# Optimization experiments

Hardware: AMD Instinct MI355X
Metric: run time of the kernel (lower is better)

The kernel has to match this reference:

```python
import jax, jax.numpy as jnp
import numpy as np

EPS = 1e-08

def quantize_weights(w):
    # absmean ternary quantization: round(w/delta) clipped to {-1,0,1}, rescaled by delta
    delta = jnp.mean(jnp.abs(w)) + EPS
    w_quant = jnp.clip(jnp.round(w / delta), -1.0, 1.0)
    return w_quant * delta

def setup_inputs() -> dict:
    key = jax.random.key(0)
    k1, k2 = jax.random.split(key)
    B, T, IN, OUT = 8, 16, 4096, 11008
    x = jax.random.normal(k1, (B, T, IN), dtype=jnp.float32)
    weight = jax.random.normal(k2, (OUT, IN), dtype=jnp.float32)
    bias = jnp.zeros((OUT,), dtype=jnp.float32)
    return {"x": x, "weight": weight, "bias": bias}

def reference(x, weight, bias):
    w_quant = quantize_weights(weight)
    # F.linear: x @ w_quant.T + bias
    out = jnp.einsum("bti,oi->bto", x, w_quant) + bias
    return out
```

## Files before the change

### kernel.cpp

```cpp
#include <hip/hip_runtime.h>
#include <hip/hip_bf16.h>

typedef __bf16 bf16x8 __attribute__((ext_vector_type(8)));
typedef float f32x4 __attribute__((ext_vector_type(4)));
typedef unsigned short ushort8 __attribute__((ext_vector_type(8)));

constexpr int M = 128;
constexpr int K = 4096;
constexpr int N = 11008;
constexpr int BN = 32;
constexpr int BK = 64;
constexpr long long NW = (long long)N * K;
constexpr int RBLK = 2048;

constexpr size_t PART_OFF = 0;
constexpr size_t XBF_OFF  = 8192;
constexpr size_t P0_OFF   = XBF_OFF + (size_t)M * K * 2;
constexpr size_t PSZ      = (size_t)M * N * sizeof(float);
constexpr size_t P1_OFF   = P0_OFF + PSZ;
constexpr size_t WS_NEED  = P1_OFF + PSZ;

__device__ __forceinline__ unsigned short f2bf_bits(float f) {
    unsigned int u = __builtin_bit_cast(unsigned int, f);
    u += 0x7FFFu + ((u >> 16) & 1u);
    return (unsigned short)(u >> 16);
}

template <bool CVT>
__global__ __launch_bounds__(256) void absmean_partial(const float* __restrict__ w,
                                                       const float* __restrict__ x,
                                                       float* __restrict__ partials,
                                                       unsigned short* __restrict__ xbf)
{
    const int gtid = blockIdx.x * blockDim.x + threadIdx.x;
    if (CVT && gtid < M * K / 8) {
        const float4* xp = (const float4*)x + (size_t)gtid * 2;
        float4 a = xp[0], b = xp[1];
        ushort8 o;
        o[0] = f2bf_bits(a.x); o[1] = f2bf_bits(a.y);
        o[2] = f2bf_bits(a.z); o[3] = f2bf_bits(a.w);
        o[4] = f2bf_bits(b.x); o[5] = f2bf_bits(b.y);
        o[6] = f2bf_bits(b.z); o[7] = f2bf_bits(b.w);
        *(ushort8*)(xbf + (size_t)gtid * 8) = o;
    }
    const int n4 = (int)(NW / 4);
    const float4* w4 = (const float4*)w;
    float s0 = 0.f, s1 = 0.f, s2 = 0.f, s3 = 0.f;
    for (int i = gtid; i < n4; i += gridDim.x * blockDim.x) {
        float4 v = w4[i];
        s0 += fabsf(v.x); s1 += fabsf(v.y); s2 += fabsf(v.z); s3 += fabsf(v.w);
    }
    float s = (s0 + s1) + (s2 + s3);
#pragma unroll
    for (int off = 32; off > 0; off >>= 1) s += __shfl_down(s, off, 64);
    __shared__ float red[4];
    if ((threadIdx.x & 63) == 0) red[threadIdx.x >> 6] = s;
    __syncthreads();
    if (threadIdx.x == 0)
        partials[blockIdx.x] = (red[0] + red[1]) + (red[2] + red[3]);
}

template <int KSTEPS, bool DIRECT>
__global__ __launch_bounds__(256) void bitlinear_gemm(
    const void* __restrict__ Xsrc, const float* __restrict__ W,
    const float* __restrict__ bias, const float* __restrict__ partials,
    float* __restrict__ dbase)
{
    constexpr int LDSW = 72;
    __shared__ __attribute__((aligned(16))) unsigned short xs[2][M * LDSW];
    __shared__ __attribute__((aligned(16))) unsigned short wsm[2][BN * LDSW];

    const int tid = threadIdx.x;
    const int lane = tid & 63;
    const int wid = tid >> 6;
    const int wm = wid >> 1;
    const int wn = wid & 1;
    const int cgrp = lane >> 4;
    const int l15 = lane & 15;
    const int n0 = blockIdx.x * BN;
    const int kk0 = DIRECT ? 0 : blockIdx.y * KSTEPS;

    const int sr = tid >> 3;
    const int sc = tid & 7;
    const int K4 = K / 4;

    const float4* wsrc = (const float4*)(W + (size_t)(n0 + sr) * K) + sc * 2;
    const unsigned short* xb = (const unsigned short*)Xsrc;
    const float4* xf = (const float4*)Xsrc;

    float4 wr0, wr1;
    ushort8 xr[4];

    auto issue = [&](int t) {
        const int g = kk0 + t;
        wr0 = wsrc[g * 16];
        wr1 = wsrc[g * 16 + 1];
#pragma unroll
        for (int it = 0; it < 4; ++it) {
            if (!DIRECT) {
                xr[it] = *(const ushort8*)(xb + (size_t)(sr + 32 * it) * K + g * BK + sc * 8);
            } else {
                const float4* xp = xf + (size_t)(sr + 32 * it) * K4 + g * 16 + sc * 2;
                float4 a = xp[0], b = xp[1];
                ushort8 o;
                o[0] = f2bf_bits(a.x); o[1] = f2bf_bits(a.y);
                o[2] = f2bf_bits(a.z); o[3] = f2bf_bits(a.w);
                o[4] = f2bf_bits(b.x); o[5] = f2bf_bits(b.y);
                o[6] = f2bf_bits(b.z); o[7] = f2bf_bits(b.w);
                xr[it] = o;
            }
        }
    };

    issue(0);

    float s = 0.f;
#pragma unroll
    for (int i = 0; i < RBLK / 256; ++i) s += partials[tid + i * 256];
#pragma unroll
    for (int off = 32; off > 0; off >>= 1) s += __shfl_down(s, off, 64);
    __shared__ float red[4];
    if (lane == 0) red[wid] = s;
    __syncthreads();
    const float delta =
        (float)((double)((red[0] + red[1]) + (red[2] + red[3])) / (double)NW + 1e-8);
    const float inv_delta = 1.0f / delta;

    auto stage = [&](int buf) {
        float wf[8] = {wr0.x, wr0.y, wr0.z, wr0.w, wr1.x, wr1.y, wr1.z, wr1.w};
        ushort8 wq;
#pragma unroll
        for (int j = 0; j < 8; ++j) {
            float q = rintf(wf[j] * inv_delta);
            q = fminf(1.f, fmaxf(-1.f, q));
            wq[j] = f2bf_bits(q);
        }
        *(ushort8*)&wsm[buf][sr * LDSW + sc * 8] = wq;
#pragma unroll
        for (int it = 0; it < 4; ++it)
            *(ushort8*)&xs[buf][(sr + 32 * it) * LDSW + sc * 8] = xr[it];
    };

    stage(0);
    __syncthreads();

    f32x4 acc[4] = {};

    for (int t = 0; t < KSTEPS; ++t) {
        const int cur = t & 1;
        if (t + 1 < KSTEPS) issue(t + 1);
#pragma unroll
        for (int ks = 0; ks < 2; ++ks) {
            const int ch = ks * 4 + cgrp;
            bf16x8 bfr = *(const bf16x8*)&wsm[cur][(wn * 16 + l15) * LDSW + ch * 8];
#pragma unroll
            for (int f = 0; f < 4; ++f) {
                bf16x8 afr = *(const bf16x8*)&xs[cur][(wm * 64 + f * 16 + l15) * LDSW + ch * 8];
                acc[f] = __builtin_amdgcn_mfma_f32_16x16x32_bf16(afr, bfr, acc[f], 0, 0, 0);
            }
        }
        if (t + 1 < KSTEPS) stage(cur ^ 1);
        __syncthreads();
    }

    float* dst = DIRECT ? dbase : dbase + (size_t)blockIdx.y * ((size_t)M * N);
    const int ocol = n0 + wn * 16 + l15;
    const float bv = DIRECT ? bias[ocol] : 0.f;
#pragma unroll
    for (int f = 0; f < 4; ++f) {
        const int mrow = wm * 64 + f * 16 + cgrp * 4;
#pragma unroll
        for (int r = 0; r < 4; ++r)
            dst[(size_t)(mrow + r) * N + ocol] = delta * acc[f][r] + bv;
    }
}

__global__ __launch_bounds__(256) void combine(const float4* __restrict__ p0,
                                               const float4* __restrict__ p1,
                                               const float* __restrict__ bias,
                                               float4* __restrict__ out)
{
    const int i4 = blockIdx.x * blockDim.x + threadIdx.x;
    constexpr int N4 = N / 4;
    if (i4 >= M * N4) return;
    const int col4 = i4 % N4;
    const float4 b = *(const float4*)(bias + col4 * 4);
    float4 a = p0[i4], c = p1[i4];
    float4 o;
    o.x = a.x + c.x + b.x; o.y = a.y + c.y + b.y;
    o.z = a.z + c.z + b.z; o.w = a.w + c.w + b.w;
    out[i4] = o;
}

extern "C" void kernel_launch(void* const* d_in, const int* in_sizes, int n_in,
                              void* d_out, int out_size, void* d_ws, size_t ws_size,
                              hipStream_t stream) {
    const float* x = (const float*)d_in[0];
    const float* w = (const float*)d_in[1];
    const float* bias = (const float*)d_in[2];
    float* out = (float*)d_out;
    float* partials = (float*)((char*)d_ws + PART_OFF);
    unsigned short* xbf = (unsigned short*)((char*)d_ws + XBF_OFF);
    float* p0 = (float*)((char*)d_ws + P0_OFF);
    float* p1 = (float*)((char*)d_ws + P1_OFF);

    if (ws_size >= WS_NEED) {
        absmean_partial<true><<<RBLK, 256, 0, stream>>>(w, x, partials, xbf);
        bitlinear_gemm<32, false><<<dim3(N / BN, 2), 256, 0, stream>>>(
            xbf, w, bias, partials, p0);
        combine<<<(M * N / 4 + 255) / 256, 256, 0, stream>>>(
            (const float4*)p0, (const float4*)p1, bias, (float4*)out);
    } else {
        absmean_partial<false><<<RBLK, 256, 0, stream>>>(w, x, partials, xbf);
        bitlinear_gemm<64, true><<<N / BN, 256, 0, stream>>>(
            x, w, bias, partials, out);
    }
}
```

Before: 75.00 us.

## Widen GEMM tile to 128 columns and use eight-way split-K with combine

```diff
diff --git a/kernel.cpp b/kernel.cpp
--- a/kernel.cpp
+++ b/kernel.cpp
@@ -4,21 +4,22 @@
 typedef __bf16 bf16x8 __attribute__((ext_vector_type(8)));
 typedef float f32x4 __attribute__((ext_vector_type(4)));
 typedef unsigned short ushort8 __attribute__((ext_vector_type(8)));
+typedef unsigned short ushort4v __attribute__((ext_vector_type(4)));
 
 constexpr int M = 128;
 constexpr int K = 4096;
 constexpr int N = 11008;
-constexpr int BN = 32;
-constexpr int BK = 64;
+constexpr int BN = 128;
+constexpr int BK = 32;
+constexpr int KSPLIT = 8;
 constexpr long long NW = (long long)N * K;
 constexpr int RBLK = 2048;
 
 constexpr size_t PART_OFF = 0;
 constexpr size_t XBF_OFF  = 8192;
-constexpr size_t P0_OFF   = XBF_OFF + (size_t)M * K * 2;
-constexpr size_t PSZ      = (size_t)M * N * sizeof(float);
-constexpr size_t P1_OFF   = P0_OFF + PSZ;
-constexpr size_t WS_NEED  = P1_OFF + PSZ;
+constexpr size_t P_OFF    = XBF_OFF + (size_t)M * K * 2;
+constexpr size_t MN       = (size_t)M * N;
+constexpr size_t WS_NEED  = P_OFF + KSPLIT * MN * sizeof(float);
 
 __device__ __forceinline__ unsigned short f2bf_bits(float f) {
     unsigned int u = __builtin_bit_cast(unsigned int, f);
@@ -60,13 +61,13 @@
         partials[blockIdx.x] = (red[0] + red[1]) + (red[2] + red[3]);
 }
 
-template <int KSTEPS, bool DIRECT>
-__global__ __launch_bounds__(256) void bitlinear_gemm(
+template <int KSTEPS, bool PRE>
+__global__ __launch_bounds__(256, 3) void bitlinear_gemm(
     const void* __restrict__ Xsrc, const float* __restrict__ W,
     const float* __restrict__ bias, const float* __restrict__ partials,
     float* __restrict__ dbase)
 {
-    constexpr int LDSW = 72;
+    constexpr int LDSW = 40;
     __shared__ __attribute__((aligned(16))) unsigned short xs[2][M * LDSW];
     __shared__ __attribute__((aligned(16))) unsigned short wsm[2][BN * LDSW];
 
@@ -78,37 +79,39 @@
     const int cgrp = lane >> 4;
     const int l15 = lane & 15;
     const int n0 = blockIdx.x * BN;
-    const int kk0 = DIRECT ? 0 : blockIdx.y * KSTEPS;
-
-    const int sr = tid >> 3;
-    const int sc = tid & 7;
+    const int kk0 = PRE ? blockIdx.y * (K / KSPLIT) : 0;
     const int K4 = K / 4;
 
-    const float4* wsrc = (const float4*)(W + (size_t)(n0 + sr) * K) + sc * 2;
     const unsigned short* xb = (const unsigned short*)Xsrc;
     const float4* xf = (const float4*)Xsrc;
-
-    float4 wr0, wr1;
-    ushort8 xr[4];
+    const float4* w4p = (const float4*)W;
+
+    ushort8 xr[2];
+    float4 wr[4];
 
     auto issue = [&](int t) {
-        const int g = kk0 + t;
-        wr0 = wsrc[g * 16];
-        wr1 = wsrc[g * 16 + 1];
-#pragma unroll
-        for (int it = 0; it < 4; ++it) {
-            if (!DIRECT) {
-                xr[it] = *(const ushort8*)(xb + (size_t)(sr + 32 * it) * K + g * BK + sc * 8);
+#pragma unroll
+        for (int i = 0; i < 2; ++i) {
+            const int j = tid + i * 256;
+            const int row = j >> 2, ch = j & 3;
+            if (PRE) {
+                xr[i] = *(const ushort8*)(xb + (size_t)row * K + kk0 + t * BK + ch * 8);
             } else {
-                const float4* xp = xf + (size_t)(sr + 32 * it) * K4 + g * 16 + sc * 2;
+                const float4* xp = xf + (size_t)row * K4 + t * (BK / 4) + ch * 2;
                 float4 a = xp[0], b = xp[1];
                 ushort8 o;
                 o[0] = f2bf_bits(a.x); o[1] = f2bf_bits(a.y);
                 o[2] = f2bf_bits(a.z); o[3] = f2bf_bits(a.w);
                 o[4] = f2bf_bits(b.x); o[5] = f2bf_bits(b.y);
                 o[6] = f2bf_bits(b.z); o[7] = f2bf_bits(b.w);
-                xr[it] = o;
+                xr[i] = o;
             }
+        }
+#pragma unroll
+        for (int i = 0; i < 4; ++i) {
+            const int j = tid + i * 256;
+            const int row = j >> 3, q = j & 7;
+            wr[i] = w4p[(size_t)(n0 + row) * K4 + kk0 / 4 + t * (BK / 4) + q];
         }
     };
 
@@ -127,69 +130,84 @@
     const float inv_delta = 1.0f / delta;
 
     auto stage = [&](int buf) {
-        float wf[8] = {wr0.x, wr0.y, wr0.z, wr0.w, wr1.x, wr1.y, wr1.z, wr1.w};
-        ushort8 wq;
-#pragma unroll
-        for (int j = 0; j < 8; ++j) {
-            float q = rintf(wf[j] * inv_delta);
-            q = fminf(1.f, fmaxf(-1.f, q));
-            wq[j] = f2bf_bits(q);
-        }
-        *(ushort8*)&wsm[buf][sr * LDSW + sc * 8] = wq;
-#pragma unroll
-        for (int it = 0; it < 4; ++it)
-            *(ushort8*)&xs[buf][(sr + 32 * it) * LDSW + sc * 8] = xr[it];
+#pragma unroll
+        for (int i = 0; i < 2; ++i) {
+            const int j = tid + i * 256;
+            *(ushort8*)&xs[buf][(j >> 2) * LDSW + (j & 3) * 8] = xr[i];
+        }
+#pragma unroll
+        for (int i = 0; i < 4; ++i) {
+            const int j = tid + i * 256;
+            const int row = j >> 3, q = j & 7;
+            float wf[4] = {wr[i].x, wr[i].y, wr[i].z, wr[i].w};
+            ushort4v wq;
+#pragma unroll
+            for (int e = 0; e < 4; ++e) {
+                float qv = rintf(wf[e] * inv_delta);
+                qv = fminf(1.f, fmaxf(-1.f, qv));
+                wq[e] = f2bf_bits(qv);
+            }
+            *(ushort4v*)&wsm[buf][row * LDSW + q * 4] = wq;
+        }
     };
 
     stage(0);
     __syncthreads();
 
-    f32x4 acc[4] = {};
+    f32x4 acc[4][4] = {};
 
     for (int t = 0; t < KSTEPS; ++t) {
         const int cur = t & 1;
         if (t + 1 < KSTEPS) issue(t + 1);
-#pragma unroll
-        for (int ks = 0; ks < 2; ++ks) {
-            const int ch = ks * 4 + cgrp;
-            bf16x8 bfr = *(const bf16x8*)&wsm[cur][(wn * 16 + l15) * LDSW + ch * 8];
-#pragma unroll
-            for (int f = 0; f < 4; ++f) {
-                bf16x8 afr = *(const bf16x8*)&xs[cur][(wm * 64 + f * 16 + l15) * LDSW + ch * 8];
-                acc[f] = __builtin_amdgcn_mfma_f32_16x16x32_bf16(afr, bfr, acc[f], 0, 0, 0);
-            }
-        }
+        const unsigned short* xcur = xs[cur];
+        const unsigned short* wcur = wsm[cur];
+        bf16x8 afr[4], bfr[4];
+#pragma unroll
+        for (int f = 0; f < 4; ++f)
+            afr[f] = *(const bf16x8*)&xcur[(wm * 64 + f * 16 + l15) * LDSW + cgrp * 8];
+#pragma unroll
+        for (int g = 0; g < 4; ++g)
+            bfr[g] = *(const bf16x8*)&wcur[(wn * 64 + g * 16 + l15) * LDSW + cgrp * 8];
+#pragma unroll
+        for (int f = 0; f < 4; ++f)
+#pragma unroll
+            for (int g = 0; g < 4; ++g)
+                acc[f][g] = __builtin_amdgcn_mfma_f32_16x16x32_bf16(
+                    afr[f], bfr[g], acc[f][g], 0, 0, 0);
         if (t + 1 < KSTEPS) stage(cur ^ 1);
         __syncthreads();
     }
 
-    float* dst = DIRECT ? dbase : dbase + (size_t)blockIdx.y * ((size_t)M * N);
-    const int ocol = n0 + wn * 16 + l15;
-    const float bv = DIRECT ? bias[ocol] : 0.f;
+    float* dst = PRE ? dbase + (size_t)blockIdx.y * MN : dbase;
 #pragma unroll
     for (int f = 0; f < 4; ++f) {
         const int mrow = wm * 64 + f * 16 + cgrp * 4;
 #pragma unroll
-        for (int r = 0; r < 4; ++r)
-            dst[(size_t)(mrow + r) * N + ocol] = delta * acc[f][r] + bv;
-    }
-}
-
-__global__ __launch_bounds__(256) void combine(const float4* __restrict__ p0,
-                                               const float4* __restrict__ p1,
+        for (int g = 0; g < 4; ++g) {
+            const int ocol = n0 + wn * 64 + g * 16 + l15;
+            const float bv = PRE ? 0.f : bias[ocol];
+#pragma unroll
+            for (int r = 0; r < 4; ++r)
+                dst[(size_t)(mrow + r) * N + ocol] = delta * acc[f][g][r] + bv;
+        }
+    }
+}
+
+__global__ __launch_bounds__(256) void combine(const float* __restrict__ p,
                                                const float* __restrict__ bias,
                                                float4* __restrict__ out)
 {
     const int i4 = blockIdx.x * blockDim.x + threadIdx.x;
     constexpr int N4 = N / 4;
-    if (i4 >= M * N4) return;
+    if (i4 >= (int)(MN / 4)) return;
     const int col4 = i4 % N4;
-    const float4 b = *(const float4*)(bias + col4 * 4);
-    float4 a = p0[i4], c = p1[i4];
-    float4 o;
-    o.x = a.x + c.x + b.x; o.y = a.y + c.y + b.y;
-    o.z = a.z + c.z + b.z; o.w = a.w + c.w + b.w;
-    out[i4] = o;
+    float4 s = *(const float4*)(bias + col4 * 4);
+#pragma unroll
+    for (int y = 0; y < KSPLIT; ++y) {
+        float4 v = ((const float4*)(p + y * MN))[i4];
+        s.x += v.x; s.y += v.y; s.z += v.z; s.w += v.w;
+    }
+    out[i4] = s;
 }
 
 extern "C" void kernel_launch(void* const* d_in, const int* in_sizes, int n_in,
@@ -201,18 +219,16 @@
     float* out = (float*)d_out;
     float* partials = (float*)((char*)d_ws + PART_OFF);
     unsigned short* xbf = (unsigned short*)((char*)d_ws + XBF_OFF);
-    float* p0 = (float*)((char*)d_ws + P0_OFF);
-    float* p1 = (float*)((char*)d_ws + P1_OFF);
+    float* pbase = (float*)((char*)d_ws + P_OFF);
 
     if (ws_size >= WS_NEED) {
         absmean_partial<true><<<RBLK, 256, 0, stream>>>(w, x, partials, xbf);
-        bitlinear_gemm<32, false><<<dim3(N / BN, 2), 256, 0, stream>>>(
-            xbf, w, bias, partials, p0);
-        combine<<<(M * N / 4 + 255) / 256, 256, 0, stream>>>(
-            (const float4*)p0, (const float4*)p1, bias, (float4*)out);
+        bitlinear_gemm<K / KSPLIT / BK, true><<<dim3(N / BN, KSPLIT), 256, 0, stream>>>(
+            xbf, w, bias, partials, pbase);
+        combine<<<(int)(MN / 4 + 255) / 256, 256, 0, stream>>>(pbase, bias, (float4*)out);
     } else {
         absmean_partial<false><<<RBLK, 256, 0, stream>>>(w, x, partials, xbf);
-        bitlinear_gemm<64, true><<<N / BN, 256, 0, stream>>>(
+        bitlinear_gemm<K / BK, false><<<dim3(N / BN, 1), 256, 0, stream>>>(
             x, w, bias, partials, out);
     }
 }
```

After: 77.32 us. 3.1% more time.
